# Optimization experiments

Hardware: AMD Instinct MI355X
Metric: run time of the kernel (lower is better)

The kernel has to match this reference:

```python
import jax, jax.numpy as jnp
import numpy as np
from jax import lax

H, W = 2048, 2048
KS = 3            # spatial NMS / centroid kernel size
EPS_NMS = 1e-5    # NMS3d eps (threshold=0 branch)
EPS_DIV = 1e-8
BORDER = 1        # int(mrSize=1.0)


def _grid_weights():
    # generate_3dgrid(3, 3, 3) centered: coords = linspace(-k/2+1, k/2, k) = [-0.5, 0.5, 1.5]
    c = np.linspace(-KS / 2 + 1, KS / 2, KS).astype(np.float32)
    g2 = np.stack([np.repeat(c, KS), np.tile(c, KS)], 1)                              # [9,2] (y,x), y-major
    g3 = np.concatenate([np.repeat(c, KS * KS)[:, None], np.tile(g2, (KS, 1))], 1)    # [27,3] (z,y,x)
    # grid.t().view(3,3,3,3): out-channel c holds coordinate c over the 3x3x3 cube (OIHW)
    return jnp.asarray(g3.T.reshape(3, 3, KS, KS))


def _border_mask():
    m = np.ones((H, W), np.float32)
    m[:BORDER] = 0; m[H - BORDER:] = 0; m[:, :BORDER] = 0; m[:, W - BORDER:] = 0
    return jnp.asarray(m)


def setup_inputs() -> dict:
    key = jax.random.key(0)
    k1, k2, k3, k4 = jax.random.split(key, 4)
    return {
        "low": jax.random.uniform(k1, (1, 1, H, W), jnp.float32),
        "cur": jax.random.uniform(k2, (1, 1, H, W), jnp.float32),
        "high": jax.random.uniform(k3, (1, 1, H, W), jnp.float32),
        "aff_resp": jax.random.normal(k4, (1, 4, H, W), jnp.float32),
        "octaveMap": jnp.zeros((1, 1, H, W), jnp.float32),
        "num_features": 4096,
    }


def _core(low, cur, high, aff_resp, octaveMap, num_features):
    resp3d = jnp.concatenate([low, cur, high], axis=1)  # [1,3,H,W] scale cube
    # MaxPool3d(kernel=3, stride=1, padding=(0,1,1)) over (scale,H,W) -> [1,1,H,W]
    mp = lax.reduce_window(resp3d, -jnp.inf, lax.max,
                           (1, 3, 3, 3), (1, 1, 1, 1),
                           [(0, 0), (0, 0), (1, 1), (1, 1)])
    nms = (resp3d - mp + EPS_NMS > 0).astype(resp3d.dtype) * resp3d  # broadcast over 3 scales
    # keep only the center scale, zero 1px border, mask already-taken octave positions
    nmsed = nms[:, 1:2] * _border_mask() * (1.0 - octaveMap)          # [1,1,H,W]
    vals, idxs = lax.top_k(nmsed.reshape(-1), num_features)          # fixed-k selection branch
    # centroid fit: coordinate-weighted 3x3x3 sums / mass via conv2d over the 3 scale channels
    gw = _grid_weights()
    num = lax.conv_general_dilated(resp3d, gw, (1, 1), [(1, 1), (1, 1)])
    den = lax.conv_general_dilated(resp3d, jnp.ones((3, 3, KS, KS), resp3d.dtype),
                                   (1, 1), [(1, 1), (1, 1)])
    sc = num / (den + EPS_DIV)  # [1,3,H,W] = (scale, dy, dx)
    yy, xx = jnp.meshgrid(jnp.arange(H, dtype=sc.dtype), jnp.arange(W, dtype=sc.dtype), indexing="ij")
    sc = jnp.stack([sc[0, 0], sc[0, 1] + yy, sc[0, 2] + xx], 0).reshape(3, -1).T  # [H*W,3]
    sc = sc[idxs] / jnp.array([float(min(H, W)), float(H), float(W)], sc.dtype)   # normalize (s,y,x)
    A = aff_resp.reshape(4, -1).T[idxs].reshape(-1, 2, 2)   # gather per-keypoint affine
    A = sc[:, 0][:, None, None] * A                          # scale * A
    center_xy = jnp.stack([sc[:, 2], sc[:, 1]], axis=1)[:, :, None]  # (x, y) column
    lafs = jnp.concatenate([A, center_xy], axis=2)           # [K,2,3] LAFs
    return vals, lafs, nmsed


def reference(low, cur, high, aff_resp, octaveMap, num_features):
    vals, lafs, nmsed = _core(low, cur, high, aff_resp, octaveMap, num_features)
    octave_new = (octaveMap + nmsed).astype(jnp.uint8)  # updated octave occupancy map
    return vals, lafs, octave_new
```

## Files before the change

kernel.cpp:

```cpp
#include <hip/hip_runtime.h>
#include <cstdint>
#include <cstddef>

#define HH 2048
#define WW 2048
#define NPIX (HH * WW)
#define EPS_NMS 1e-5f
#define EPS_DIV 1e-8f
#define NEG_INF (-3.402823466e+38f)
#define ROWS 8
#define LCAP 2048
#define SBUF_CAP 256
#define SG_CAP 7680
#define NBIN 2048
#define RANK_BLOCKS 512
#define CREW 64
#define RB_ELEMS 64
#define BUFCAP 1024
#define T0F 0.99854f

typedef unsigned long long u64;


__device__ __forceinline__ float max3(float a, float b, float c) {
    return fmaxf(a, fmaxf(b, c));
}

__device__ __forceinline__ unsigned int aload(const unsigned int* p) {
    return __hip_atomic_load(p, __ATOMIC_RELAXED, __HIP_MEMORY_SCOPE_AGENT);
}

__device__ __forceinline__ void gbar(char* base, unsigned int crewid) {
    __syncthreads();
    if (threadIdx.x == 0) {
        unsigned int* root = (unsigned int*)base;
        unsigned int* gc = (unsigned int*)(base + 64 + ((crewid & 7u) << 6));
        __threadfence();
        if (atomicAdd(gc, 1u) == 7u) atomicAdd(root, 1u);
        while (aload(root) < 8u) __builtin_amdgcn_s_sleep(1);
        __threadfence();
    }
    __syncthreads();
}

__device__ __forceinline__ void pick_bin(const unsigned int* __restrict__ hg,
                                         unsigned int remk_in,
                                         unsigned int* s,
                                         unsigned int* sh_bin,
                                         unsigned int* sh_rem)
{
    const int tid = threadIdx.x;
    unsigned int bins[8], csum = 0;
    #pragma unroll
    for (int i = 0; i < 8; ++i) { bins[i] = aload(&hg[tid * 8 + i]); csum += bins[i]; }
    s[tid] = csum;
    __syncthreads();
    for (int off = 1; off < 256; off <<= 1) {
        unsigned int v = (tid + off < 256) ? s[tid + off] : 0u;
        __syncthreads(); s[tid] += v; __syncthreads();
    }
    unsigned int incl = s[tid], excl = incl - csum, total = s[0];
    if (tid == 0 && total < remk_in) { *sh_bin = 0u; *sh_rem = remk_in; }
    if (incl >= remk_in && excl < remk_in) {
        unsigned int cum = excl; int b = 7;
        for (; b > 0; --b) { cum += bins[b]; if (cum >= remk_in) break; }
        if (cum < remk_in) cum += bins[0];
        *sh_bin = (unsigned int)(tid * 8 + b);
        *sh_rem = remk_in - (cum - bins[b]);
    }
    __syncthreads();
}

__device__ __forceinline__ void finalize_key(
    u64 my_key, unsigned int rank,
    const float* __restrict__ low, const float* __restrict__ cur,
    const float* __restrict__ high, const float* __restrict__ aff,
    float* __restrict__ out, int K)
{
    float val = __uint_as_float((unsigned int)(my_key >> 32));
    unsigned int idx = ~((unsigned int)my_key);
    out[rank] = val;
    float* laf = out + K + (size_t)rank * 6;
    int y = (int)(idx >> 11), x = (int)(idx & (WW - 1));
    const float ccw[3] = {-0.5f, 0.5f, 1.5f};
    float den = 0.0f, nz = 0.0f, ny = 0.0f, nx = 0.0f;
    #pragma unroll
    for (int dy = -1; dy <= 1; ++dy) {
        int yy = y + dy;
        if (yy < 0 || yy >= HH) continue;
        #pragma unroll
        for (int dx = -1; dx <= 1; ++dx) {
            int xx = x + dx;
            if (xx < 0 || xx >= WW) continue;
            int jj = yy * WW + xx;
            float v0 = low[jj], v1 = cur[jj], v2 = high[jj];
            float ssum = v0 + v1 + v2;
            den += ssum;
            nz += -0.5f * v0 + 0.5f * v1 + 1.5f * v2;
            ny += ccw[dy + 1] * ssum;
            nx += ccw[dx + 1] * ssum;
        }
    }
    float inv = 1.0f / (den + EPS_DIV);
    float s_n = (nz * inv) * (1.0f / 2048.0f);
    float y_n = (ny * inv + (float)y) * (1.0f / 2048.0f);
    float x_n = (nx * inv + (float)x) * (1.0f / 2048.0f);
    float a0 = aff[idx], a1 = aff[NPIX + idx];
    float a2 = aff[2 * NPIX + idx], a3 = aff[3 * NPIX + idx];
    laf[0] = s_n * a0; laf[1] = s_n * a1; laf[2] = x_n;
    laf[3] = s_n * a2; laf[4] = s_n * a3; laf[5] = y_n;
}

__global__ __launch_bounds__(256) void nms_map_kernel(
    const float* __restrict__ low, const float* __restrict__ cur,
    const float* __restrict__ high, const float* __restrict__ oct,
    float* __restrict__ oct_out, float* __restrict__ vals_out, int n7k,
    u64* __restrict__ cand, unsigned int* __restrict__ cnt,
    u64* __restrict__ SG, unsigned int cap)
{
    __shared__ unsigned int lcount, lbase, lT, lsb;
    __shared__ u64 lcand[LCAP];
    __shared__ u64 sbuf[SBUF_CAP];

    const int tid = threadIdx.x;
    const int lane = tid & 63;
    const int x4 = blockIdx.x * 1024 + tid * 4;
    const int y0 = blockIdx.y * ROWS;
    if (tid == 0) { lcount = 0u; lT = 0u; }

    if (blockIdx.y == 0) {
        int n4 = n7k >> 2;
        float4* vz = (float4*)vals_out;
        for (int i = blockIdx.x * 256 + tid; i < n4; i += gridDim.x * 256)
            vz[i] = make_float4(0.f, 0.f, 0.f, 0.f);
    }
    __syncthreads();

    float4 Lb[6], Cb[6], Hb[6], Ob[4];
    float eLl[6], eLc[6], eLh[6], eRl[6], eRc[6], eRh[6];

    #define ISSUE(r) {                                                            \
        const int sl = (r) % 6;                                                   \
        int tt = y0 - 1 + (r);                                                    \
        if (tt >= 0 && tt < HH) {                                                 \
            int jj = tt * WW + x4;                                                \
            Lb[sl] = *(const float4*)(low  + jj);                                 \
            Cb[sl] = *(const float4*)(cur  + jj);                                 \
            Hb[sl] = *(const float4*)(high + jj);                                 \
            bool doL = (lane == 0)  && (x4 > 0);                                  \
            bool doR = (lane == 63) && (x4 + 4 < WW);                             \
            eLl[sl] = doL ? low[jj - 1]  : NEG_INF;                               \
            eLc[sl] = doL ? cur[jj - 1]  : NEG_INF;                               \
            eLh[sl] = doL ? high[jj - 1] : NEG_INF;                               \
            eRl[sl] = doR ? low[jj + 4]  : NEG_INF;                               \
            eRc[sl] = doR ? cur[jj + 4]  : NEG_INF;                               \
            eRh[sl] = doR ? high[jj + 4] : NEG_INF;                               \
        } else {                                                                  \
            Lb[sl] = Cb[sl] = Hb[sl] =                                            \
                make_float4(NEG_INF, NEG_INF, NEG_INF, NEG_INF);                  \
            eLl[sl] = eLc[sl] = eLh[sl] = NEG_INF;                                \
            eRl[sl] = eRc[sl] = eRh[sl] = NEG_INF;                                \
        }                                                                         \
    }

    #define CONSUME(r, hzO) {                                                     \
        const int sl = (r) % 6;                                                   \
        float4 l = Lb[sl], c = Cb[sl], hh = Hb[sl];                               \
        float4 z;                                                                 \
        z.x = max3(l.x, c.x, hh.x);                                               \
        z.y = max3(l.y, c.y, hh.y);                                               \
        z.z = max3(l.z, c.z, hh.z);                                               \
        z.w = max3(l.w, c.w, hh.w);                                               \
        float zeL = max3(eLl[sl], eLc[sl], eLh[sl]);                              \
        float zeR = max3(eRl[sl], eRc[sl], eRh[sl]);                              \
        float zl = __shfl_up(z.w, 1, 64);                                         \
        float zr = __shfl_down(z.x, 1, 64);                                       \
        if (lane == 0)  zl = zeL;                                                 \
        if (lane == 63) zr = zeR;                                                 \
        hzO.x = max3(zl,  z.x, z.y);                                              \
        hzO.y = max3(z.x, z.y, z.z);                                              \
        hzO.z = max3(z.y, z.z, z.w);                                              \
        hzO.w = max3(z.z, z.w, zr);                                               \
    }

    float4 hzA, hzB, hzC;
    ISSUE(0) ISSUE(1) ISSUE(2) ISSUE(3) ISSUE(4)
    Ob[0] = *(const float4*)(oct + (y0 + 0) * WW + x4);
    Ob[1] = *(const float4*)(oct + (y0 + 1) * WW + x4);
    Ob[2] = *(const float4*)(oct + (y0 + 2) * WW + x4);
    CONSUME(0, hzA)
    CONSUME(1, hzB)

    #pragma unroll
    for (int j = 0; j < ROWS; ++j) {
        int y = y0 + j;
        if (j + 5 <= 9) ISSUE(j + 5)
        if (j + 3 < ROWS)
            Ob[(j + 3) & 3] = *(const float4*)(oct + (y + 3) * WW + x4);
        CONSUME(j + 2, hzC)

        int idx = y * WW + x4;
        float4 o = Ob[j & 3];
        float4 cv = Cb[(j + 1) % 6];
        bool yin = (y > 0) && (y < HH - 1);
        float4 ov;
        #define DO_COMP(comp, i)  {                                               \
            float m = max3(hzA.comp, hzB.comp, hzC.comp);                         \
            int xg = x4 + (i);                                                    \
            bool interior = yin && (xg > 0) && (xg < WW - 1);                     \
            float nm = (((cv.comp - m + EPS_NMS) > 0.0f) && interior)             \
                       ? cv.comp * (1.0f - o.comp) : 0.0f;                        \
            ov.comp = (float)((unsigned char)(o.comp + nm));                      \
            if (nm > 0.0f) {                                                      \
                unsigned int p = atomicAdd(&lcount, 1u);                          \
                if (p < LCAP)                                                     \
                    lcand[p] = (((u64)__float_as_uint(nm)) << 32)                 \
                               | (unsigned int)(~(idx + (i)));                    \
            }                                                                     \
        }
        DO_COMP(x, 0) DO_COMP(y, 1) DO_COMP(z, 2) DO_COMP(w, 3)
        #undef DO_COMP
        *(float4*)(oct_out + idx) = ov;
        hzA = hzB; hzB = hzC;
    }
    #undef ISSUE
    #undef CONSUME

    __syncthreads();
    unsigned int c = lcount < LCAP ? lcount : LCAP;
    if (tid == 0) lbase = atomicAdd(&cnt[0], c);
    __syncthreads();
    unsigned int base = lbase;
    const u64 T0KEY = ((u64)__float_as_uint(T0F)) << 32;
    for (unsigned int i = tid; i < c; i += 256) {
        u64 k = lcand[i];
        unsigned int p = base + i;
        if (p < cap) cand[p] = k;
        if (k >= T0KEY) {
            unsigned int q = atomicAdd(&lT, 1u);
            if (q < SBUF_CAP) sbuf[q] = k;
        }
    }
    __syncthreads();
    unsigned int t = lT;
    if (tid == 0) {
        if (t > (unsigned int)SBUF_CAP) atomicExch(&cnt[4], 1u);
        lsb = t ? atomicAdd(&cnt[5], t) : 0u;
    }
    __syncthreads();
    unsigned int nb = t < (unsigned int)SBUF_CAP ? t : (unsigned int)SBUF_CAP;
    unsigned int sb = lsb;
    for (unsigned int i = tid; i < nb; i += 256) {
        unsigned int p = sb + i;
        if (p < (unsigned int)SG_CAP) SG[p] = sbuf[i];
    }
}

__global__ __launch_bounds__(256) void rank_kernel(
    const u64* __restrict__ cand, u64* __restrict__ SG,
    unsigned int* __restrict__ cnt,
    unsigned int* __restrict__ hist0, unsigned int* __restrict__ hist1,
    unsigned int cap, int K,
    const float* __restrict__ low, const float* __restrict__ cur,
    const float* __restrict__ high, const float* __restrict__ aff,
    float* __restrict__ out)
{
    __shared__ u64 sgl[SG_CAP];
    __shared__ unsigned int s[256];
    __shared__ unsigned int rnk[RB_ELEMS];
    __shared__ unsigned int sh_bin, sh_rem, lc, lb;
    unsigned int* h = (unsigned int*)sgl;
    u64* buf = sgl + 2048;

    const int tid = threadIdx.x;
    const int bid = blockIdx.x;
    const unsigned int wave = (unsigned int)tid >> 6, ln = (unsigned int)tid & 63u;

    unsigned int m = cnt[5];
    bool fast = (cnt[4] == 0u) && (m >= (unsigned int)K) && (m <= (unsigned int)SG_CAP);

    if (fast) {
        for (unsigned int i = tid; i < m; i += 256) sgl[i] = SG[i];
        __syncthreads();

        unsigned int g = (unsigned int)bid * 4u + wave;
        u64 my[4];
        unsigned int r[4];
        #pragma unroll
        for (int j = 0; j < 4; ++j) {
            unsigned int i = g + 2048u * (unsigned int)j;
            my[j] = (i < m) ? sgl[i] : ~0ull;
            r[j] = 0u;
        }
        for (unsigned int j2 = ln; j2 < m; j2 += 64) {
            u64 key = sgl[j2];
            #pragma unroll
            for (int j = 0; j < 4; ++j) r[j] += (unsigned int)(key > my[j]);
        }
        #pragma unroll
        for (int j = 0; j < 4; ++j) {
            #pragma unroll
            for (int off = 32; off > 0; off >>= 1)
                r[j] += __shfl_down(r[j], off, 64);
            if (ln == 0) rnk[wave * 4 + j] = r[j];
        }
        __syncthreads();

        if (tid < 16) {
            unsigned int w2 = (unsigned int)tid >> 2, j = (unsigned int)tid & 3u;
            unsigned int i = (unsigned int)bid * 4u + w2 + 2048u * j;
            if (i < m) {
                unsigned int rank = rnk[w2 * 4 + j];
                if (rank < (unsigned int)K)
                    finalize_key(sgl[i], rank, low, cur, high, aff, out, K);
            }
        }
        return;
    }

    if (bid >= CREW) return;
    const unsigned int crewid = (unsigned int)bid;
    char* barb = (char*)cnt + 128;
    unsigned int n0 = cnt[0];
    unsigned int n = n0; if (n > cap) n = cap;
    const unsigned int stride = CREW * 256;

    for (int i = tid; i < NBIN; i += 256) h[i] = 0u;
    __syncthreads();
    for (unsigned int i = crewid * 256 + tid; i < n; i += stride)
        atomicAdd(&h[(unsigned int)(cand[i] >> 53)], 1u);
    __syncthreads();
    for (int i = tid; i < NBIN; i += 256) { unsigned int v = h[i]; if (v) atomicAdd(&hist0[i], v); }
    gbar(barb, crewid);
    pick_bin(hist0, (unsigned int)K, s, &sh_bin, &sh_rem);
    const unsigned int prefix = sh_bin;
    const unsigned int remk   = sh_rem;

    for (int i = tid; i < NBIN; i += 256) h[i] = 0u;
    __syncthreads();
    for (unsigned int i = crewid * 256 + tid; i < n; i += stride) {
        unsigned int k32 = (unsigned int)(cand[i] >> 32);
        if ((k32 >> 21) == prefix) atomicAdd(&h[(k32 >> 10) & (NBIN - 1u)], 1u);
    }
    __syncthreads();
    for (int i = tid; i < NBIN; i += 256) { unsigned int v = h[i]; if (v) atomicAdd(&hist1[i], v); }
    gbar(barb + 576, crewid);
    pick_bin(hist1, remk, s, &sh_bin, &sh_rem);
    const unsigned int T = (prefix << 11) | sh_bin;

    if (tid == 0) lc = 0u;
    __syncthreads();
    for (unsigned int i = crewid * 256 + tid; i < n; i += stride) {
        u64 key = cand[i];
        if ((unsigned int)(key >> 42) >= T) {
            unsigned int p = atomicAdd(&lc, 1u);
            if (p < BUFCAP) buf[p] = key;
        }
    }
    __syncthreads();
    unsigned int cc = lc < BUFCAP ? lc : BUFCAP;
    if (tid == 0) lb = atomicAdd(&cnt[1], cc);
    __syncthreads();
    unsigned int b2 = lb;
    for (unsigned int i = tid; i < cc; i += 256) {
        unsigned int p = b2 + i;
        if (p < (unsigned int)SG_CAP) SG[p] = buf[i];
    }
    gbar(barb + 2 * 576, crewid);
    unsigned int m2 = aload(&cnt[1]); if (m2 > (unsigned int)SG_CAP) m2 = SG_CAP;

    for (unsigned int i = tid; i < m2; i += 256) sgl[i] = SG[i];
    __syncthreads();
    for (unsigned int chunk = crewid * RB_ELEMS; chunk < m2;
         chunk += (unsigned int)CREW * RB_ELEMS) {
        u64 my[16];
        unsigned int r[16];
        #pragma unroll
        for (int i = 0; i < 16; ++i) {
            unsigned int e = chunk + wave * 16 + i;
            my[i] = (e < m2) ? sgl[e] : ~0ull;
            r[i] = 0u;
        }
        for (unsigned int j = ln; j < m2; j += 64) {
            u64 key = sgl[j];
            #pragma unroll
            for (int i = 0; i < 16; ++i) r[i] += (unsigned int)(key > my[i]);
        }
        #pragma unroll
        for (int i = 0; i < 16; ++i) {
            #pragma unroll
            for (int off = 32; off > 0; off >>= 1)
                r[i] += __shfl_down(r[i], off, 64);
            if (ln == 0) rnk[wave * 16 + i] = r[i];
        }
        __syncthreads();
        if (tid < RB_ELEMS) {
            unsigned int e = chunk + (unsigned int)tid;
            if (e < m2) {
                unsigned int rank = rnk[tid];
                if (rank < (unsigned int)K)
                    finalize_key(sgl[e], rank, low, cur, high, aff, out, K);
            }
        }
        __syncthreads();
    }
}

extern "C" void kernel_launch(void* const* d_in, const int* in_sizes, int n_in,
                              void* d_out, int out_size, void* d_ws, size_t ws_size,
                              hipStream_t stream) {
    const float* low  = (const float*)d_in[0];
    const float* cur  = (const float*)d_in[1];
    const float* high = (const float*)d_in[2];
    const float* aff  = (const float*)d_in[3];
    const float* oct  = (const float*)d_in[4];
    int K = (out_size - NPIX) / 7;
    float* out = (float*)d_out;

    char* ws = (char*)d_ws;
    unsigned int* cnt   = (unsigned int*)ws;
    unsigned int* hist0 = (unsigned int*)(ws + 4096);
    unsigned int* hist1 = (unsigned int*)(ws + 12288);
    u64* SG             = (u64*)(ws + 20480);
    const size_t cand_off = 98304;
    u64* cand           = (u64*)(ws + cand_off);
    size_t cap_sz = ws_size > cand_off ? (ws_size - cand_off) / 8 : 0;
    if (cap_sz > (size_t)NPIX) cap_sz = (size_t)NPIX;
    unsigned int cap = (unsigned int)cap_sz;

    hipMemsetAsync(ws, 0, 20480, stream);

    dim3 gb(WW / 1024, HH / ROWS, 1);
    nms_map_kernel<<<gb, 256, 0, stream>>>(low, cur, high, oct,
                                           out + (size_t)7 * K, out, 7 * K,
                                           cand, cnt, SG, cap);
    rank_kernel<<<RANK_BLOCKS, 256, 0, stream>>>(cand, SG, cnt, hist0, hist1,
                                                 cap, K, low, cur, high, aff, out);
}
```

Measured before the change: 178.7 us.

## Rank 64 candidates per block with fewer rank blocks and early exit

The fast ranking path now assigns 64 contiguous candidates per block (16 per wave) instead of 16 strided ones. RANK_BLOCKS drops from 512 to 128, and blocks whose slice lies beyond the candidate count exit before loading shared memory. This cuts the number of blocks that each copy the full candidate list into LDS and reuses every loaded key across more comparisons. In exchange it raises register pressure and per-block serial work, and it only covers up to 8192 candidates, which still fits within SG_CAP.

```diff
diff --git a/kernel.cpp b/kernel.cpp
--- a/kernel.cpp
+++ b/kernel.cpp
@@ -13,7 +13,7 @@
 #define SBUF_CAP 256
 #define SG_CAP 7680
 #define NBIN 2048
-#define RANK_BLOCKS 512
+#define RANK_BLOCKS 128
 #define CREW 64
 #define RB_ELEMS 64
 #define BUFCAP 1024
@@ -280,39 +280,39 @@
     bool fast = (cnt[4] == 0u) && (m >= (unsigned int)K) && (m <= (unsigned int)SG_CAP);
 
     if (fast) {
+        unsigned int kbase = (unsigned int)bid * RB_ELEMS;
+        if (kbase >= m) return;
         for (unsigned int i = tid; i < m; i += 256) sgl[i] = SG[i];
         __syncthreads();
 
-        unsigned int g = (unsigned int)bid * 4u + wave;
-        u64 my[4];
-        unsigned int r[4];
+        u64 my[16];
+        unsigned int r[16];
         #pragma unroll
-        for (int j = 0; j < 4; ++j) {
-            unsigned int i = g + 2048u * (unsigned int)j;
-            my[j] = (i < m) ? sgl[i] : ~0ull;
-            r[j] = 0u;
+        for (int i = 0; i < 16; ++i) {
+            unsigned int e = kbase + wave * 16u + (unsigned int)i;
+            my[i] = (e < m) ? sgl[e] : ~0ull;
+            r[i] = 0u;
         }
         for (unsigned int j2 = ln; j2 < m; j2 += 64) {
             u64 key = sgl[j2];
             #pragma unroll
-            for (int j = 0; j < 4; ++j) r[j] += (unsigned int)(key > my[j]);
+            for (int i = 0; i < 16; ++i) r[i] += (unsigned int)(key > my[i]);
         }
         #pragma unroll
-        for (int j = 0; j < 4; ++j) {
+        for (int i = 0; i < 16; ++i) {
             #pragma unroll
             for (int off = 32; off > 0; off >>= 1)
-                r[j] += __shfl_down(r[j], off, 64);
-            if (ln == 0) rnk[wave * 4 + j] = r[j];
+                r[i] += __shfl_down(r[i], off, 64);
+            if (ln == 0) rnk[wave * 16 + i] = r[i];
         }
         __syncthreads();
 
-        if (tid < 16) {
-            unsigned int w2 = (unsigned int)tid >> 2, j = (unsigned int)tid & 3u;
-            unsigned int i = (unsigned int)bid * 4u + w2 + 2048u * j;
-            if (i < m) {
-                unsigned int rank = rnk[w2 * 4 + j];
+        if (tid < RB_ELEMS) {
+            unsigned int e = kbase + (unsigned int)tid;
+            if (e < m) {
+                unsigned int rank = rnk[tid];
                 if (rank < (unsigned int)K)
-                    finalize_key(sgl[i], rank, low, cur, high, aff, out, K);
+                    finalize_key(sgl[e], rank, low, cur, high, aff, out, K);
             }
         }
         return;
```

After: 191.1 us. +6.9%, slower.
